# Performance work log

Measured on AMD Instinct MI355X. Metric: run time of the kernel, lower is better.

Reference implementation:

```python
import jax, jax.numpy as jnp
import numpy as np
import math

H = 1024
E = 16
ENT_STRENGTH = 0.5
COHERENCE_TIME = 10.0
TIME_STEP = 0.0
K = 2
# static list of rotation pairs (i<j), applied sequentially as in the torch double loop
PAIRS = np.array([(i, j) for i in range(E) for j in range(i + 1, E)], dtype=np.int32)


def _mlp(x, w1, b1, w2, b2):
    h = jax.nn.gelu(x @ w1 + b1, approximate=False)  # torch default GELU = exact erf
    return h @ w2 + b2


def _apply_entanglement(amps, ent):
    # sequential Givens rotations over expert pairs; carry shape [B,S,E]
    pairs = jnp.asarray(PAIRS)

    def step(carry, pair):
        i, j = pair[0], pair[1]
        angle = ent[i, j] * ENT_STRENGTH
        c, s = jnp.cos(angle), jnp.sin(angle)
        ai = jnp.take(carry, i, axis=-1)  # [B,S]
        aj = jnp.take(carry, j, axis=-1)
        oh_i = jax.nn.one_hot(i, E, dtype=carry.dtype)
        oh_j = jax.nn.one_hot(j, E, dtype=carry.dtype)
        new = (carry * (1.0 - oh_i - oh_j)
               + (c * ai - s * aj)[..., None] * oh_i
               + (s * ai + c * aj)[..., None] * oh_j)
        return new, None

    out, _ = jax.lax.scan(step, amps, pairs)
    return out


def setup_inputs() -> dict:
    key = jax.random.key(0)
    ks = jax.random.split(key, 10)
    sc1 = 1.0 / math.sqrt(H)
    sc2 = 1.0 / math.sqrt(H // 2)
    return {
        "hidden_states": jax.random.normal(ks[0], (4, 4096, H), dtype=jnp.float32),
        "w1a": jax.random.uniform(ks[1], (H, H // 2), jnp.float32, -sc1, sc1),
        "b1a": jnp.zeros((H // 2,), jnp.float32),
        "w2a": jax.random.uniform(ks[2], (H // 2, E), jnp.float32, -sc2, sc2),
        "b2a": jnp.zeros((E,), jnp.float32),
        "w1p": jax.random.uniform(ks[3], (H, H // 2), jnp.float32, -sc1, sc1),
        "b1p": jnp.zeros((H // 2,), jnp.float32),
        "w2p": jax.random.uniform(ks[4], (H // 2, E), jnp.float32, -sc2, sc2),
        "b2p": jnp.zeros((E,), jnp.float32),
        "ent": jax.random.normal(ks[5], (E, E), dtype=jnp.float32) * 0.1,
    }


def reference(hidden_states, w1a, b1a, w2a, b2a, w1p, b1p, w2p, b2p, ent):
    raw_amps = _mlp(hidden_states, w1a, b1a, w2a, b2a)                 # [B,S,E]
    raw_phases = jnp.tanh(_mlp(hidden_states, w1p, b1p, w2p, b2p)) * jnp.float32(math.pi)
    amplitudes = jnp.sqrt(jax.nn.softmax(jnp.abs(raw_amps), axis=-1))
    entangled = _apply_entanglement(amplitudes, ent)
    coherence = jnp.exp(jnp.float32(-TIME_STEP / COHERENCE_TIME))      # time_step buffer = 0 -> 1.0
    decoherent = entangled * coherence
    probs = decoherent ** 2
    probs = probs / jnp.maximum(jnp.sum(jnp.abs(probs), axis=-1, keepdims=True), 1e-12)
    top_p, top_i = jax.lax.top_k(probs, K)
    top_p = top_p / jnp.maximum(jnp.sum(jnp.abs(top_p), axis=-1, keepdims=True), 1e-12)
    return top_p, top_i, decoherent, raw_phases, probs
```

## Files before the change

kernel.cpp:

```cpp
#include <hip/hip_runtime.h>
#include <math.h>

#define NTOK   16384
#define HDIM   1024
#define HHALF  512
#define NE     16

#define OFF_TP  0
#define OFF_TI  (NTOK * 2)
#define OFF_DEC (NTOK * 4)
#define OFF_PH  (OFF_DEC + NTOK * NE)
#define OFF_PR  (OFF_PH + NTOK * NE)

typedef _Float16 half8 __attribute__((ext_vector_type(8)));
typedef _Float16 half4 __attribute__((ext_vector_type(4)));
typedef float f32x16 __attribute__((ext_vector_type(16)));
typedef float f32x4 __attribute__((ext_vector_type(4)));

#define LO_SCALE     2048.0f
#define LO_SCALE_INV (1.0f / 2048.0f)
#define MFMA32(a,b,c) __builtin_amdgcn_mfma_f32_32x32x16_f16(a,b,c,0,0,0)
#define MFMA16(a,b,c) __builtin_amdgcn_mfma_f32_16x16x32_f16(a,b,c,0,0,0)

#define BAR() asm volatile("s_waitcnt lgkmcnt(0)\n\ts_barrier" ::: "memory")

__device__ __forceinline__ float gelu_exact(float x) {
    return 0.5f * x * (1.0f + erff(x * 0.70710678118654752440f));
}

__device__ __forceinline__ void cvt_split(float4 v, half4& hi, half4& lo) {
    _Float16 h0 = (_Float16)v.x, h1 = (_Float16)v.y,
             h2 = (_Float16)v.z, h3 = (_Float16)v.w;
    hi = (half4){h0, h1, h2, h3};
    lo = (half4){(_Float16)((v.x - (float)h0) * LO_SCALE),
                 (_Float16)((v.y - (float)h1) * LO_SCALE),
                 (_Float16)((v.z - (float)h2) * LO_SCALE),
                 (_Float16)((v.w - (float)h3) * LO_SCALE)};
}

__global__ void __launch_bounds__(256)
qir_wtrans(const float* __restrict__ w1a, const float* __restrict__ w1p,
           _Float16* __restrict__ wt, float* __restrict__ out)
{
    int u = blockIdx.x * 256 + threadIdx.x;
    out[OFF_PH + u] = 0.0f;
    out[OFF_PH + 262144 + u] = 0.0f;

    int l  = u & 63;
    int f  = (u >> 6) & 7;
    int sl = (u >> 9) & 7;
    int kc = (u >> 12) & 31;
    int ph = u >> 17;
    int nf = f >> 2, kh = (f >> 1) & 1, pl = f & 1;
    int col = sl * 64 + nf * 32 + (l & 31);
    int k0  = kc * 32 + kh * 16 + (l >> 5) * 8;
    const float* __restrict__ W = ph ? w1p : w1a;
    half8 v;
    #pragma unroll
    for (int j = 0; j < 8; ++j) {
        float x = W[(size_t)(k0 + j) * HHALF + col];
        _Float16 h = (_Float16)x;
        v[j] = pl ? (_Float16)((x - (float)h) * LO_SCALE) : h;
    }
    *(half8*)&wt[(size_t)u * 8] = v;
}

__device__ __forceinline__ void kstep(
    int kc, const float* __restrict__ aptr, const _Float16* __restrict__ bptr,
    char* Acur, char* Anxt, int a_rd, int a_off0, int a_off1,
    half8 (&Bc)[4], half8 (&Bn)[4],
    float4 (&xw)[2], float4 (&xl)[2],
    f32x16 (&am)[4], f32x16 (&cm)[4])
{
    if (kc + 2 < 32) {
        xl[0] = *(const float4*)(aptr + (kc + 2) * 32);
        xl[1] = *(const float4*)(aptr + (kc + 2) * 32 + 16);
    }
    if (kc + 1 < 32) {
        #pragma unroll
        for (int j = 0; j < 4; ++j)
            Bn[j] = *(const half8*)(bptr + (size_t)(kc + 1) * 32768 + j * 512);
    }
    #pragma unroll
    for (int kh = 0; kh < 2; ++kh) {
        const char* Ah = Acur + kh * 4096 + a_rd;
        half8 ah[4], al[4];
        #pragma unroll
        for (int mf = 0; mf < 4; ++mf) {
            ah[mf] = *(const half8*)(Ah + mf * 512);
            al[mf] = *(const half8*)(Ah + 8192 + mf * 512);
        }
        half8 bh = Bc[kh * 2], bl = Bc[kh * 2 + 1];
        #pragma unroll
        for (int mf = 0; mf < 4; ++mf) {
            am[mf] = MFMA32(ah[mf], bh, am[mf]);
            cm[mf] = MFMA32(al[mf], bh, cm[mf]);
            cm[mf] = MFMA32(ah[mf], bl, cm[mf]);
        }
    }
    if (kc + 1 < 32) {
        half4 hv, lv;
        cvt_split(xw[0], hv, lv);
        *(half4*)(Anxt + a_off0) = hv; *(half4*)(Anxt + a_off0 + 8192) = lv;
        cvt_split(xw[1], hv, lv);
        *(half4*)(Anxt + a_off1) = hv; *(half4*)(Anxt + a_off1 + 8192) = lv;
    }
    BAR();
}

__global__ void __launch_bounds__(512, 2)
qir_gemm(const float* __restrict__ xg, const _Float16* __restrict__ wt,
         const float* __restrict__ b1a, const float* __restrict__ w2a, const float* __restrict__ b2a,
         const float* __restrict__ b1p, const float* __restrict__ w2p, const float* __restrict__ b2p,
         float* __restrict__ out)
{
    extern __shared__ char smem[];
    const int tid = threadIdx.x;
    const int l  = tid & 63;
    const int w  = tid >> 6;
    const int bid  = blockIdx.x;
    const int mblk = bid & 127;
    const int v    = bid >> 7;
    const int ph   = v & 1;
    const int nh   = v >> 1;
    const int tok0 = mblk * 128;

    const float* __restrict__ b1 = ph ? b1p : b1a;
    const float* __restrict__ w2 = ph ? w2p : w2a;
    const float* __restrict__ b2 = ph ? b2p : b2a;
    const _Float16* __restrict__ wtp = wt + ((size_t)ph << 20);

    char* const Ab0 = smem;
    char* const Ab1 = smem + 16384;

    const int r  = tid >> 2;
    const int kq = tid & 3;
    const float* __restrict__ aptr = xg + (size_t)(tok0 + r) * HDIM + kq * 4;
    const int a_off0 = (kq >> 1) * 2048 + r * 16 + (kq & 1) * 8;
    const int a_off1 = a_off0 + 4096;
    const int a_rd = (l >> 5) * 2048 + (l & 31) * 16;

    const int c32 = nh * 8 + w;
    const _Float16* __restrict__ bptr =
        wtp + (c32 >> 1) * 4096 + (c32 & 1) * 2048 + (size_t)l * 8;

    f32x16 am[4], cm[4];
    #pragma unroll
    for (int mf = 0; mf < 4; ++mf)
        #pragma unroll
        for (int rg = 0; rg < 16; ++rg) { am[mf][rg] = 0.f; cm[mf][rg] = 0.f; }

    half8 Bc[4], Bn[4];
    float4 xw[2], xl[2];

    {
        float4 v0 = *(const float4*)(aptr);
        float4 v1 = *(const float4*)(aptr + 16);
        half4 hv, lv;
        cvt_split(v0, hv, lv);
        *(half4*)(Ab0 + a_off0) = hv; *(half4*)(Ab0 + a_off0 + 8192) = lv;
        cvt_split(v1, hv, lv);
        *(half4*)(Ab0 + a_off1) = hv; *(half4*)(Ab0 + a_off1 + 8192) = lv;
    }
    #pragma unroll
    for (int j = 0; j < 4; ++j) Bc[j] = *(const half8*)(bptr + j * 512);
    xw[0] = *(const float4*)(aptr + 32);
    xw[1] = *(const float4*)(aptr + 48);
    BAR();

    for (int kk = 0; kk < 16; ++kk) {
        kstep(2 * kk,     aptr, bptr, Ab0, Ab1, a_rd, a_off0, a_off1,
              Bc, Bn, xw, xl, am, cm);
        kstep(2 * kk + 1, aptr, bptr, Ab1, Ab0, a_rd, a_off0, a_off1,
              Bn, Bc, xl, xw, am, cm);
    }

    const float bb = b1[nh * 256 + w * 32 + (l & 31)];
    #pragma unroll
    for (int mf = 0; mf < 4; ++mf)
        #pragma unroll
        for (int rg = 0; rg < 16; ++rg)
            am[mf][rg] = gelu_exact(am[mf][rg] + cm[mf][rg] * LO_SCALE_INV + bb);

    char* const Hw = smem + w * 5120;

    half8 w2h, w2l;
    #pragma unroll
    for (int j = 0; j < 8; ++j) {
        int kg = nh * 256 + w * 32 + (l >> 4) * 8 + j;
        float vv = w2[(size_t)kg * NE + (l & 15)];
        _Float16 hh = (_Float16)vv;
        w2h[j] = hh;
        w2l[j] = (_Float16)((vv - (float)hh) * LO_SCALE);
    }

    f32x4 acc2[2][4], acc2s[2][4];
    #pragma unroll
    for (int p2 = 0; p2 < 2; ++p2)
        #pragma unroll
        for (int m16 = 0; m16 < 4; ++m16)
            #pragma unroll
            for (int rg = 0; rg < 4; ++rg) { acc2[p2][m16][rg] = 0.f; acc2s[p2][m16][rg] = 0.f; }

    #pragma unroll
    for (int p2 = 0; p2 < 2; ++p2) {
        #pragma unroll
        for (int fr = 0; fr < 2; ++fr)
            #pragma unroll
            for (int rg = 0; rg < 16; ++rg) {
                int row = fr * 32 + (rg & 3) + 8 * (rg >> 2) + 4 * (l >> 5);
                float vv = am[p2 * 2 + fr][rg];
                *(_Float16*)(Hw + row * 80 + (l & 31) * 2) = (_Float16)vv;
            }
        #pragma unroll
        for (int m16 = 0; m16 < 4; ++m16) {
            half8 a2 = *(const half8*)(Hw + (m16 * 16 + (l & 15)) * 80 + (l >> 4) * 16);
            acc2[p2][m16]  = MFMA16(a2, w2h, acc2[p2][m16]);
            acc2s[p2][m16] = MFMA16(a2, w2l, acc2s[p2][m16]);
        }
        #pragma unroll
        for (int fr = 0; fr < 2; ++fr)
            #pragma unroll
            for (int rg = 0; rg < 16; ++rg) {
                int row = fr * 32 + (rg & 3) + 8 * (rg >> 2) + 4 * (l >> 5);
                float vv = am[p2 * 2 + fr][rg];
                _Float16 hh = (_Float16)vv;
                *(_Float16*)(Hw + row * 80 + (l & 31) * 2) = (_Float16)(vv - (float)hh);
            }
        #pragma unroll
        for (int m16 = 0; m16 < 4; ++m16) {
            half8 a2 = *(const half8*)(Hw + (m16 * 16 + (l & 15)) * 80 + (l >> 4) * 16);
            acc2[p2][m16] = MFMA16(a2, w2h, acc2[p2][m16]);
        }
    }

    __syncthreads();
    float* const P = (float*)smem;
    #pragma unroll
    for (int p2 = 0; p2 < 2; ++p2)
        #pragma unroll
        for (int m16 = 0; m16 < 4; ++m16)
            #pragma unroll
            for (int rg = 0; rg < 4; ++rg) {
                int t = p2 * 64 + m16 * 16 + ((l >> 4) << 2) + rg;
                P[w * 2048 + t * 16 + (l & 15)] =
                    acc2[p2][m16][rg] + acc2s[p2][m16][rg] * LO_SCALE_INV;
            }
    __syncthreads();

    #pragma unroll
    for (int rep = 0; rep < 4; ++rep) {
        int oi = tid + rep * 512;
        int t = oi >> 4, e = oi & 15;
        float sum = 0.5f * b2[e];
        #pragma unroll
        for (int w8 = 0; w8 < 8; ++w8) sum += P[w8 * 2048 + t * 16 + e];
        atomicAdd(out + (ph ? OFF_PH : OFF_PR) + (size_t)(tok0 + t) * NE + e, sum);
    }
}

__global__ void __launch_bounds__(512)
qir_mlp(const float* __restrict__ xg,
        const float* __restrict__ w1a, const float* __restrict__ b1a,
        const float* __restrict__ w2a, const float* __restrict__ b2a,
        const float* __restrict__ w1p, const float* __restrict__ b1p,
        const float* __restrict__ w2p, const float* __restrict__ b2p,
        float* __restrict__ out)
{
    __shared__ float sh_w[16][HHALF];
    __shared__ float sh_x[16][68];

    const int tid  = threadIdx.x;
    const int cg   = tid & 63;
    const int tg   = tid >> 6;
    const int tok0 = blockIdx.x * 64;
    const int cA   = cg * 4;
    const int cB   = 256 + cg * 4;

    for (int phase = 0; phase < 2; ++phase) {
        const float* __restrict__ w1 = phase ? w1p : w1a;
        const float* __restrict__ b1 = phase ? b1p : b1a;
        const float* __restrict__ w2 = phase ? w2p : w2a;
        const float* __restrict__ b2 = phase ? b2p : b2a;

        float acc[8][8];
        #pragma unroll
        for (int t = 0; t < 8; ++t)
            #pragma unroll
            for (int c = 0; c < 8; ++c) acc[t][c] = 0.0f;

        float4 wreg[4];
        float4 xreg = make_float4(0.f, 0.f, 0.f, 0.f);

        auto load_chunk = [&](int kc) {
            #pragma unroll
            for (int p = 0; p < 4; ++p) {
                int f  = tid + p * 512;
                int k  = f >> 7;
                int c4 = (f & 127) << 2;
                wreg[p] = *(const float4*)&w1[(kc * 16 + k) * HHALF + c4];
            }
            if (tid < 256) {
                int t  = tid >> 2;
                int k4 = (tid & 3) << 2;
                xreg = *(const float4*)&xg[(size_t)(tok0 + t) * HDIM + kc * 16 + k4];
            }
        };

        load_chunk(0);
        for (int kc = 0; kc < HDIM / 16; ++kc) {
            __syncthreads();
            #pragma unroll
            for (int p = 0; p < 4; ++p) {
                int f  = tid + p * 512;
                int k  = f >> 7;
                int c4 = (f & 127) << 2;
                *(float4*)&sh_w[k][c4] = wreg[p];
            }
            if (tid < 256) {
                int t  = tid >> 2;
                int k4 = (tid & 3) << 2;
                sh_x[k4 + 0][t] = xreg.x;
                sh_x[k4 + 1][t] = xreg.y;
                sh_x[k4 + 2][t] = xreg.z;
                sh_x[k4 + 3][t] = xreg.w;
            }
            __syncthreads();
            if (kc + 1 < HDIM / 16) load_chunk(kc + 1);

            #pragma unroll 4
            for (int k = 0; k < 16; ++k) {
                float4 xa = *(const float4*)&sh_x[k][tg * 8];
                float4 xb = *(const float4*)&sh_x[k][tg * 8 + 4];
                float4 wa = *(const float4*)&sh_w[k][cA];
                float4 wb = *(const float4*)&sh_w[k][cB];
                float xs[8] = {xa.x, xa.y, xa.z, xa.w, xb.x, xb.y, xb.z, xb.w};
                float ws[8] = {wa.x, wa.y, wa.z, wa.w, wb.x, wb.y, wb.z, wb.w};
                #pragma unroll
                for (int t = 0; t < 8; ++t)
                    #pragma unroll
                    for (int c = 0; c < 8; ++c)
                        acc[t][c] = fmaf(xs[t], ws[c], acc[t][c]);
            }
        }

        {
            float4 bA4 = *(const float4*)&b1[cA];
            float4 bB4 = *(const float4*)&b1[cB];
            float bs[8] = {bA4.x, bA4.y, bA4.z, bA4.w, bB4.x, bB4.y, bB4.z, bB4.w};
            #pragma unroll
            for (int t = 0; t < 8; ++t)
                #pragma unroll
                for (int c = 0; c < 8; ++c)
                    acc[t][c] = gelu_exact(acc[t][c] + bs[c]);
        }

        for (int e = 0; e < NE; ++e) {
            float w2v[8];
            #pragma unroll
            for (int j = 0; j < 4; ++j) {
                w2v[j]     = w2[(cA + j) * NE + e];
                w2v[4 + j] = w2[(cB + j) * NE + e];
            }
            float bias2 = b2[e];
            #pragma unroll
            for (int t = 0; t < 8; ++t) {
                float s = 0.0f;
                #pragma unroll
                for (int j = 0; j < 8; ++j) s = fmaf(acc[t][j], w2v[j], s);
                #pragma unroll
                for (int off = 1; off < 64; off <<= 1)
                    s += __shfl_xor(s, off, 64);
                if (cg == 0) {
                    float raw   = s + bias2;
                    int   token = tok0 + tg * 8 + t;
                    out[(phase ? OFF_PH : OFF_PR) + (size_t)token * NE + e] = raw;
                }
            }
        }
    }
}

__global__ void __launch_bounds__(256)
qir_epilogue(const float* __restrict__ ent, float* __restrict__ out)
{
    __shared__ float sh_c[120], sh_s[120];
    const int tid = threadIdx.x;
    if (tid < 120) {
        int rem = tid, i = 0;
        while (rem >= 15 - i) { rem -= 15 - i; ++i; }
        int j = i + 1 + rem;
        float ang = ent[i * NE + j] * 0.5f;
        sh_c[tid] = cosf(ang);
        sh_s[tid] = sinf(ang);
    }
    __syncthreads();

    const int token = blockIdx.x * 256 + tid;

    #pragma unroll
    for (int q = 0; q < 4; ++q) {
        float4 v = *(const float4*)&out[OFF_PH + (size_t)token * NE + q * 4];
        v.x = tanhf(v.x) * 3.14159265358979323846f;
        v.y = tanhf(v.y) * 3.14159265358979323846f;
        v.z = tanhf(v.z) * 3.14159265358979323846f;
        v.w = tanhf(v.w) * 3.14159265358979323846f;
        *(float4*)&out[OFF_PH + (size_t)token * NE + q * 4] = v;
    }

    float a[16];
    #pragma unroll
    for (int q = 0; q < 4; ++q) {
        float4 v = *(const float4*)&out[OFF_PR + (size_t)token * NE + q * 4];
        a[q*4+0] = v.x; a[q*4+1] = v.y; a[q*4+2] = v.z; a[q*4+3] = v.w;
    }

    float m = fabsf(a[0]);
    #pragma unroll
    for (int e = 1; e < 16; ++e) m = fmaxf(m, fabsf(a[e]));
    float ssum = 0.0f;
    #pragma unroll
    for (int e = 0; e < 16; ++e) { a[e] = expf(fabsf(a[e]) - m); ssum += a[e]; }
    float inv = 1.0f / ssum;
    #pragma unroll
    for (int e = 0; e < 16; ++e) a[e] = sqrtf(a[e] * inv);

    {
        int p = 0;
        #pragma unroll
        for (int i = 0; i < 16; ++i) {
            #pragma unroll
            for (int j = i + 1; j < 16; ++j) {
                float c = sh_c[p], s = sh_s[p]; ++p;
                float ai = a[i], aj = a[j];
                a[i] = c * ai - s * aj;
                a[j] = s * ai + c * aj;
            }
        }
    }

    #pragma unroll
    for (int q = 0; q < 4; ++q)
        *(float4*)&out[OFF_DEC + (size_t)token * NE + q * 4] =
            make_float4(a[q*4], a[q*4+1], a[q*4+2], a[q*4+3]);

    float pr[16];
    float s2 = 0.0f;
    #pragma unroll
    for (int e = 0; e < 16; ++e) { pr[e] = a[e] * a[e]; s2 += pr[e]; }
    float inv2 = 1.0f / fmaxf(s2, 1e-12f);
    #pragma unroll
    for (int e = 0; e < 16; ++e) pr[e] *= inv2;
    #pragma unroll
    for (int q = 0; q < 4; ++q)
        *(float4*)&out[OFF_PR + (size_t)token * NE + q * 4] =
            make_float4(pr[q*4], pr[q*4+1], pr[q*4+2], pr[q*4+3]);

    float bv = pr[0]; int bi = 0;
    #pragma unroll
    for (int e = 1; e < 16; ++e) if (pr[e] > bv) { bv = pr[e]; bi = e; }
    float sv = -1.0f; int si = 0;
    #pragma unroll
    for (int e = 0; e < 16; ++e) if (e != bi && pr[e] > sv) { sv = pr[e]; si = e; }
    float ts = fmaxf(fabsf(bv) + fabsf(sv), 1e-12f);
    out[OFF_TP + (size_t)token * 2 + 0] = bv / ts;
    out[OFF_TP + (size_t)token * 2 + 1] = sv / ts;
    out[OFF_TI + (size_t)token * 2 + 0] = (float)bi;
    out[OFF_TI + (size_t)token * 2 + 1] = (float)si;
}

extern "C" void kernel_launch(void* const* d_in, const int* in_sizes, int n_in,
                              void* d_out, int out_size, void* d_ws, size_t ws_size,
                              hipStream_t stream) {
    const float* xg  = (const float*)d_in[0];
    const float* w1a = (const float*)d_in[1];
    const float* b1a = (const float*)d_in[2];
    const float* w2a = (const float*)d_in[3];
    const float* b2a = (const float*)d_in[4];
    const float* w1p = (const float*)d_in[5];
    const float* b1p = (const float*)d_in[6];
    const float* w2p = (const float*)d_in[7];
    const float* b2p = (const float*)d_in[8];
    const float* ent = (const float*)d_in[9];
    float* out = (float*)d_out;

    if (ws_size >= (size_t)4 * 1024 * 1024) {
        _Float16* wt = (_Float16*)d_ws;
        qir_wtrans<<<1024, 256, 0, stream>>>(w1a, w1p, wt, out);
        qir_gemm<<<512, 512, 65536, stream>>>(xg, wt, b1a, w2a, b2a,
                                              b1p, w2p, b2p, out);
    } else {
        qir_mlp<<<NTOK / 64, 512, 0, stream>>>(xg, w1a, b1a, w2a, b2a,
                                               w1p, b1p, w2p, b2p, out);
    }
    qir_epilogue<<<NTOK / 256, 256, 0, stream>>>(ent, out);
}
```

Baseline: 120.8 us.

## Fuse epilogue into GEMM with full-N tiles and bf16 low-part split

The GEMM is reorganised so each block covers 32 tokens and the full 512-wide hidden dimension of one MLP branch. This removes the N-split, the atomicAdd reduction, the zero-init pass and the separate epilogue kernel; softmax, the Givens rotations, normalisation and top-2 now run inside the GEMM block. The fp32 emulation also changes: the weight low part is stored as bf16 and accumulated into a single scaled accumulator, rather than kept in a separate correction accumulator. In exchange, only 32 threads per block do the serial epilogue, and the new mixed f16/bf16 split may change accuracy.

After: 137.0 us. 1.13x slower.

```diff
diff --git a/kernel.cpp b/kernel.cpp
--- a/kernel.cpp
+++ b/kernel.cpp
@@ -5,6 +5,7 @@
 #define HDIM   1024
 #define HHALF  512
 #define NE     16
+#define PI_F   3.14159265358979323846f
 
 #define OFF_TP  0
 #define OFF_TI  (NTOK * 2)
@@ -14,38 +15,33 @@
 
 typedef _Float16 half8 __attribute__((ext_vector_type(8)));
 typedef _Float16 half4 __attribute__((ext_vector_type(4)));
+typedef short    bf8   __attribute__((ext_vector_type(8)));
+typedef short    bf4   __attribute__((ext_vector_type(4)));
 typedef float f32x16 __attribute__((ext_vector_type(16)));
 typedef float f32x4 __attribute__((ext_vector_type(4)));
 
-#define LO_SCALE     2048.0f
-#define LO_SCALE_INV (1.0f / 2048.0f)
-#define MFMA32(a,b,c) __builtin_amdgcn_mfma_f32_32x32x16_f16(a,b,c,0,0,0)
-#define MFMA16(a,b,c) __builtin_amdgcn_mfma_f32_16x16x32_f16(a,b,c,0,0,0)
+#define SCALE      2048.0f
+#define SCALE_INV  (1.0f / 2048.0f)
+#define MFMA_F16(a,b,c)  __builtin_amdgcn_mfma_f32_32x32x16_f16(a,b,c,0,0,0)
+#define MFMA_BF16(a,b,c) __builtin_amdgcn_mfma_f32_32x32x16_bf16(a,b,c,0,0,0)
+#define MFMA16(a,b,c)    __builtin_amdgcn_mfma_f32_16x16x32_f16(a,b,c,0,0,0)
 
 #define BAR() asm volatile("s_waitcnt lgkmcnt(0)\n\ts_barrier" ::: "memory")
 
 __device__ __forceinline__ float gelu_exact(float x) {
     return 0.5f * x * (1.0f + erff(x * 0.70710678118654752440f));
 }
-
-__device__ __forceinline__ void cvt_split(float4 v, half4& hi, half4& lo) {
-    _Float16 h0 = (_Float16)v.x, h1 = (_Float16)v.y,
-             h2 = (_Float16)v.z, h3 = (_Float16)v.w;
-    hi = (half4){h0, h1, h2, h3};
-    lo = (half4){(_Float16)((v.x - (float)h0) * LO_SCALE),
-                 (_Float16)((v.y - (float)h1) * LO_SCALE),
-                 (_Float16)((v.z - (float)h2) * LO_SCALE),
-                 (_Float16)((v.w - (float)h3) * LO_SCALE)};
+__device__ __forceinline__ short f32_to_bf16_bits(float f) {
+    unsigned u = __builtin_bit_cast(unsigned, f);
+    u += 0x7FFFu + ((u >> 16) & 1u);
+    return (short)(u >> 16);
 }
 
 __global__ void __launch_bounds__(256)
 qir_wtrans(const float* __restrict__ w1a, const float* __restrict__ w1p,
-           _Float16* __restrict__ wt, float* __restrict__ out)
+           short* __restrict__ wt)
 {
     int u = blockIdx.x * 256 + threadIdx.x;
-    out[OFF_PH + u] = 0.0f;
-    out[OFF_PH + 262144 + u] = 0.0f;
-
     int l  = u & 63;
     int f  = (u >> 6) & 7;
     int sl = (u >> 9) & 7;
@@ -55,207 +51,284 @@
     int col = sl * 64 + nf * 32 + (l & 31);
     int k0  = kc * 32 + kh * 16 + (l >> 5) * 8;
     const float* __restrict__ W = ph ? w1p : w1a;
-    half8 v;
+    bf8 v;
     #pragma unroll
     for (int j = 0; j < 8; ++j) {
         float x = W[(size_t)(k0 + j) * HHALF + col];
         _Float16 h = (_Float16)x;
-        v[j] = pl ? (_Float16)((x - (float)h) * LO_SCALE) : h;
-    }
-    *(half8*)&wt[(size_t)u * 8] = v;
-}
-
-__device__ __forceinline__ void kstep(
-    int kc, const float* __restrict__ aptr, const _Float16* __restrict__ bptr,
-    char* Acur, char* Anxt, int a_rd, int a_off0, int a_off1,
-    half8 (&Bc)[4], half8 (&Bn)[4],
-    float4 (&xw)[2], float4 (&xl)[2],
-    f32x16 (&am)[4], f32x16 (&cm)[4])
-{
-    if (kc + 2 < 32) {
-        xl[0] = *(const float4*)(aptr + (kc + 2) * 32);
-        xl[1] = *(const float4*)(aptr + (kc + 2) * 32 + 16);
-    }
-    if (kc + 1 < 32) {
-        #pragma unroll
-        for (int j = 0; j < 4; ++j)
-            Bn[j] = *(const half8*)(bptr + (size_t)(kc + 1) * 32768 + j * 512);
-    }
-    #pragma unroll
-    for (int kh = 0; kh < 2; ++kh) {
-        const char* Ah = Acur + kh * 4096 + a_rd;
-        half8 ah[4], al[4];
-        #pragma unroll
-        for (int mf = 0; mf < 4; ++mf) {
-            ah[mf] = *(const half8*)(Ah + mf * 512);
-            al[mf] = *(const half8*)(Ah + 8192 + mf * 512);
-        }
-        half8 bh = Bc[kh * 2], bl = Bc[kh * 2 + 1];
-        #pragma unroll
-        for (int mf = 0; mf < 4; ++mf) {
-            am[mf] = MFMA32(ah[mf], bh, am[mf]);
-            cm[mf] = MFMA32(al[mf], bh, cm[mf]);
-            cm[mf] = MFMA32(ah[mf], bl, cm[mf]);
-        }
-    }
-    if (kc + 1 < 32) {
-        half4 hv, lv;
-        cvt_split(xw[0], hv, lv);
-        *(half4*)(Anxt + a_off0) = hv; *(half4*)(Anxt + a_off0 + 8192) = lv;
-        cvt_split(xw[1], hv, lv);
-        *(half4*)(Anxt + a_off1) = hv; *(half4*)(Anxt + a_off1 + 8192) = lv;
-    }
-    BAR();
-}
-
-__global__ void __launch_bounds__(512, 2)
-qir_gemm(const float* __restrict__ xg, const _Float16* __restrict__ wt,
+        v[j] = pl ? f32_to_bf16_bits(x - (float)h)
+                  : __builtin_bit_cast(short, h);
+    }
+    *(bf8*)&wt[(size_t)u * 8] = v;
+}
+
+__global__ void __launch_bounds__(256, 2)
+qir_gemm(const float* __restrict__ xg, const short* __restrict__ wt,
          const float* __restrict__ b1a, const float* __restrict__ w2a, const float* __restrict__ b2a,
          const float* __restrict__ b1p, const float* __restrict__ w2p, const float* __restrict__ b2p,
-         float* __restrict__ out)
+         const float* __restrict__ ent, float* __restrict__ out)
 {
     extern __shared__ char smem[];
     const int tid = threadIdx.x;
     const int l  = tid & 63;
     const int w  = tid >> 6;
     const int bid  = blockIdx.x;
-    const int mblk = bid & 127;
-    const int v    = bid >> 7;
-    const int ph   = v & 1;
-    const int nh   = v >> 1;
-    const int tok0 = mblk * 128;
+    const int mblk = bid & 511;
+    const int ph   = bid >> 9;
+    const int tok0 = mblk * 32;
 
     const float* __restrict__ b1 = ph ? b1p : b1a;
     const float* __restrict__ w2 = ph ? w2p : w2a;
     const float* __restrict__ b2 = ph ? b2p : b2a;
-    const _Float16* __restrict__ wtp = wt + ((size_t)ph << 20);
+    const short* __restrict__ wtp = wt + ((size_t)ph << 20);
+
+    float* const cs = (float*)(smem + 16384);
+    float* const sn = cs + 120;
+    if (tid < 120) {
+        int rem = tid, i = 0;
+        while (rem >= 15 - i) { rem -= 15 - i; ++i; }
+        int j = i + 1 + rem;
+        float ang = ent[i * NE + j] * 0.5f;
+        cs[tid] = cosf(ang);
+        sn[tid] = sinf(ang);
+    }
+
+    const int r  = tid >> 3;
+    const int kq = tid & 7;
+    const float* __restrict__ aptr = xg + (size_t)(tok0 + r) * HDIM + kq * 4;
+    const int a_w  = ((kq >> 2) * 2 + ((kq >> 1) & 1)) * 3 * 512 + r * 16 + (kq & 1) * 8;
+    const int a_rd = (l >> 5) * 3 * 512 + (l & 31) * 16;
+
+    f32x16 acc[4];
+    #pragma unroll
+    for (int g = 0; g < 4; ++g)
+        #pragma unroll
+        for (int rg = 0; rg < 16; ++rg) acc[g][rg] = 0.0f;
+
+    half8 Bch[4], Bdh[4];
+    bf8   Bcl[4], Bdl[4];
+    float4 xw, xl4;
+
+#define BOFF(KC, KH, G, PL) \
+    ((((size_t)((KC) * 8 + (2 * w + ((G) >> 1))) * 8) + ((G) & 1) * 4 + (KH) * 2 + (PL)) * 512 + (size_t)l * 8)
+
+    auto stageA = [&](char* buf, float4 v) {
+        _Float16 h0 = (_Float16)v.x, h1 = (_Float16)v.y,
+                 h2 = (_Float16)v.z, h3 = (_Float16)v.w;
+        const _Float16 S = (_Float16)SCALE;
+        half4 hi = {(_Float16)(h0 * S), (_Float16)(h1 * S),
+                    (_Float16)(h2 * S), (_Float16)(h3 * S)};
+        half4 lo = {(_Float16)((v.x - (float)h0) * SCALE),
+                    (_Float16)((v.y - (float)h1) * SCALE),
+                    (_Float16)((v.z - (float)h2) * SCALE),
+                    (_Float16)((v.w - (float)h3) * SCALE)};
+        bf4 hb = {f32_to_bf16_bits((float)h0 * SCALE),
+                  f32_to_bf16_bits((float)h1 * SCALE),
+                  f32_to_bf16_bits((float)h2 * SCALE),
+                  f32_to_bf16_bits((float)h3 * SCALE)};
+        *(half4*)(buf + a_w)        = hi;
+        *(half4*)(buf + a_w + 512)  = lo;
+        *(bf4*)  (buf + a_w + 1024) = hb;
+    };
 
     char* const Ab0 = smem;
-    char* const Ab1 = smem + 16384;
-
-    const int r  = tid >> 2;
-    const int kq = tid & 3;
-    const float* __restrict__ aptr = xg + (size_t)(tok0 + r) * HDIM + kq * 4;
-    const int a_off0 = (kq >> 1) * 2048 + r * 16 + (kq & 1) * 8;
-    const int a_off1 = a_off0 + 4096;
-    const int a_rd = (l >> 5) * 2048 + (l & 31) * 16;
-
-    const int c32 = nh * 8 + w;
-    const _Float16* __restrict__ bptr =
-        wtp + (c32 >> 1) * 4096 + (c32 & 1) * 2048 + (size_t)l * 8;
-
-    f32x16 am[4], cm[4];
-    #pragma unroll
-    for (int mf = 0; mf < 4; ++mf)
-        #pragma unroll
-        for (int rg = 0; rg < 16; ++rg) { am[mf][rg] = 0.f; cm[mf][rg] = 0.f; }
-
-    half8 Bc[4], Bn[4];
-    float4 xw[2], xl[2];
-
-    {
-        float4 v0 = *(const float4*)(aptr);
-        float4 v1 = *(const float4*)(aptr + 16);
-        half4 hv, lv;
-        cvt_split(v0, hv, lv);
-        *(half4*)(Ab0 + a_off0) = hv; *(half4*)(Ab0 + a_off0 + 8192) = lv;
-        cvt_split(v1, hv, lv);
-        *(half4*)(Ab0 + a_off1) = hv; *(half4*)(Ab0 + a_off1 + 8192) = lv;
-    }
-    #pragma unroll
-    for (int j = 0; j < 4; ++j) Bc[j] = *(const half8*)(bptr + j * 512);
-    xw[0] = *(const float4*)(aptr + 32);
-    xw[1] = *(const float4*)(aptr + 48);
+    char* const Ab1 = smem + 6144;
+
+    stageA(Ab0, *(const float4*)aptr);
+    #pragma unroll
+    for (int g = 0; g < 4; ++g) {
+        Bch[g] = *(const half8*)&wtp[BOFF(0, 0, g, 0)];
+        Bcl[g] = *(const bf8*)  &wtp[BOFF(0, 0, g, 1)];
+    }
+    xw = *(const float4*)(aptr + 32);
     BAR();
 
+    auto kstep = [&](int kc, char* Acur, char* Anxt, float4& xcur, float4& xnxt) {
+        #pragma unroll
+        for (int g = 0; g < 4; ++g) {
+            Bdh[g] = *(const half8*)&wtp[BOFF(kc, 1, g, 0)];
+            Bdl[g] = *(const bf8*)  &wtp[BOFF(kc, 1, g, 1)];
+        }
+        if (kc + 2 < 32) xnxt = *(const float4*)(aptr + (kc + 2) * 32);
+
+        {
+            const char* A0 = Acur + a_rd;
+            half8 xh = *(const half8*)(A0);
+            half8 xl = *(const half8*)(A0 + 512);
+            bf8   xb = *(const bf8*)  (A0 + 1024);
+            #pragma unroll
+            for (int g = 0; g < 4; ++g) {
+                acc[g] = MFMA_F16(xh, Bch[g], acc[g]);
+                acc[g] = MFMA_F16(xl, Bch[g], acc[g]);
+                acc[g] = MFMA_BF16(xb, Bcl[g], acc[g]);
+            }
+        }
+        if (kc + 1 < 32) {
+            #pragma unroll
+            for (int g = 0; g < 4; ++g) {
+                Bch[g] = *(const half8*)&wtp[BOFF(kc + 1, 0, g, 0)];
+                Bcl[g] = *(const bf8*)  &wtp[BOFF(kc + 1, 0, g, 1)];
+            }
+        }
+        {
+            const char* A1 = Acur + 3072 + a_rd;
+            half8 xh = *(const half8*)(A1);
+            half8 xl = *(const half8*)(A1 + 512);
+            bf8   xb = *(const bf8*)  (A1 + 1024);
+            #pragma unroll
+            for (int g = 0; g < 4; ++g) {
+                acc[g] = MFMA_F16(xh, Bdh[g], acc[g]);
+                acc[g] = MFMA_F16(xl, Bdh[g], acc[g]);
+                acc[g] = MFMA_BF16(xb, Bdl[g], acc[g]);
+            }
+        }
+        if (kc + 1 < 32) stageA(Anxt, xcur);
+        BAR();
+    };
+
     for (int kk = 0; kk < 16; ++kk) {
-        kstep(2 * kk,     aptr, bptr, Ab0, Ab1, a_rd, a_off0, a_off1,
-              Bc, Bn, xw, xl, am, cm);
-        kstep(2 * kk + 1, aptr, bptr, Ab1, Ab0, a_rd, a_off0, a_off1,
-              Bn, Bc, xl, xw, am, cm);
-    }
-
-    const float bb = b1[nh * 256 + w * 32 + (l & 31)];
-    #pragma unroll
-    for (int mf = 0; mf < 4; ++mf)
+        kstep(2 * kk,     Ab0, Ab1, xw, xl4);
+        kstep(2 * kk + 1, Ab1, Ab0, xl4, xw);
+    }
+#undef BOFF
+
+    #pragma unroll
+    for (int g = 0; g < 4; ++g) {
+        const float bb = b1[w * 128 + g * 32 + (l & 31)];
         #pragma unroll
         for (int rg = 0; rg < 16; ++rg)
-            am[mf][rg] = gelu_exact(am[mf][rg] + cm[mf][rg] * LO_SCALE_INV + bb);
-
-    char* const Hw = smem + w * 5120;
-
-    half8 w2h, w2l;
-    #pragma unroll
-    for (int j = 0; j < 8; ++j) {
-        int kg = nh * 256 + w * 32 + (l >> 4) * 8 + j;
-        float vv = w2[(size_t)kg * NE + (l & 15)];
-        _Float16 hh = (_Float16)vv;
-        w2h[j] = hh;
-        w2l[j] = (_Float16)((vv - (float)hh) * LO_SCALE);
-    }
-
-    f32x4 acc2[2][4], acc2s[2][4];
-    #pragma unroll
-    for (int p2 = 0; p2 < 2; ++p2)
-        #pragma unroll
-        for (int m16 = 0; m16 < 4; ++m16)
-            #pragma unroll
-            for (int rg = 0; rg < 4; ++rg) { acc2[p2][m16][rg] = 0.f; acc2s[p2][m16][rg] = 0.f; }
-
-    #pragma unroll
-    for (int p2 = 0; p2 < 2; ++p2) {
-        #pragma unroll
-        for (int fr = 0; fr < 2; ++fr)
-            #pragma unroll
-            for (int rg = 0; rg < 16; ++rg) {
-                int row = fr * 32 + (rg & 3) + 8 * (rg >> 2) + 4 * (l >> 5);
-                float vv = am[p2 * 2 + fr][rg];
-                *(_Float16*)(Hw + row * 80 + (l & 31) * 2) = (_Float16)vv;
-            }
-        #pragma unroll
-        for (int m16 = 0; m16 < 4; ++m16) {
-            half8 a2 = *(const half8*)(Hw + (m16 * 16 + (l & 15)) * 80 + (l >> 4) * 16);
-            acc2[p2][m16]  = MFMA16(a2, w2h, acc2[p2][m16]);
-            acc2s[p2][m16] = MFMA16(a2, w2l, acc2s[p2][m16]);
-        }
-        #pragma unroll
-        for (int fr = 0; fr < 2; ++fr)
-            #pragma unroll
-            for (int rg = 0; rg < 16; ++rg) {
-                int row = fr * 32 + (rg & 3) + 8 * (rg >> 2) + 4 * (l >> 5);
-                float vv = am[p2 * 2 + fr][rg];
-                _Float16 hh = (_Float16)vv;
-                *(_Float16*)(Hw + row * 80 + (l & 31) * 2) = (_Float16)(vv - (float)hh);
-            }
-        #pragma unroll
-        for (int m16 = 0; m16 < 4; ++m16) {
-            half8 a2 = *(const half8*)(Hw + (m16 * 16 + (l & 15)) * 80 + (l >> 4) * 16);
-            acc2[p2][m16] = MFMA16(a2, w2h, acc2[p2][m16]);
-        }
-    }
-
+            acc[g][rg] = gelu_exact(acc[g][rg] * SCALE_INV + bb);
+    }
+
+    char* const Hw = smem + w * 2048;
+    char* const hb = Hw + ((l >> 3) & 3) * 512 + (l & 7) * 2;
+    float* const P = (float*)(smem + 8192);
+
+    f32x4 acc2[2], acc2s[2];
+    #pragma unroll
+    for (int m16 = 0; m16 < 2; ++m16)
+        #pragma unroll
+        for (int rg = 0; rg < 4; ++rg) { acc2[m16][rg] = 0.f; acc2s[m16][rg] = 0.f; }
+
+    #pragma unroll
+    for (int g = 0; g < 4; ++g) {
+        half8 w2h, w2l;
+        #pragma unroll
+        for (int j = 0; j < 8; ++j) {
+            int kg = w * 128 + g * 32 + (l >> 4) * 8 + j;
+            float vv = w2[(size_t)kg * NE + (l & 15)];
+            _Float16 hh = (_Float16)vv;
+            w2h[j] = hh;
+            w2l[j] = (_Float16)((vv - (float)hh) * SCALE);
+        }
+        #pragma unroll
+        for (int rg = 0; rg < 16; ++rg) {
+            int row0 = (rg & 3) + 8 * (rg >> 2) + 4 * (l >> 5);
+            *(_Float16*)(hb + row0 * 16) = (_Float16)acc[g][rg];
+        }
+        #pragma unroll
+        for (int m16 = 0; m16 < 2; ++m16) {
+            half8 a2 = *(const half8*)(Hw + (l >> 4) * 512 +
+                                       (m16 * 16 + (l & 15)) * 16);
+            acc2[m16]  = MFMA16(a2, w2h, acc2[m16]);
+            acc2s[m16] = MFMA16(a2, w2l, acc2s[m16]);
+        }
+        #pragma unroll
+        for (int rg = 0; rg < 16; ++rg) {
+            int row0 = (rg & 3) + 8 * (rg >> 2) + 4 * (l >> 5);
+            float vv = acc[g][rg];
+            _Float16 hh = (_Float16)vv;
+            *(_Float16*)(hb + row0 * 16) = (_Float16)(vv - (float)hh);
+        }
+        #pragma unroll
+        for (int m16 = 0; m16 < 2; ++m16) {
+            half8 a2 = *(const half8*)(Hw + (l >> 4) * 512 +
+                                       (m16 * 16 + (l & 15)) * 16);
+            acc2[m16] = MFMA16(a2, w2h, acc2[m16]);
+        }
+    }
+
+    #pragma unroll
+    for (int m16 = 0; m16 < 2; ++m16)
+        #pragma unroll
+        for (int rg = 0; rg < 4; ++rg) {
+            int row = m16 * 16 + ((l >> 4) << 2) + rg;
+            P[w * 512 + row * 16 + (l & 15)] =
+                acc2[m16][rg] + acc2s[m16][rg] * SCALE_INV;
+        }
     __syncthreads();
-    float* const P = (float*)smem;
-    #pragma unroll
-    for (int p2 = 0; p2 < 2; ++p2)
-        #pragma unroll
-        for (int m16 = 0; m16 < 4; ++m16)
-            #pragma unroll
-            for (int rg = 0; rg < 4; ++rg) {
-                int t = p2 * 64 + m16 * 16 + ((l >> 4) << 2) + rg;
-                P[w * 2048 + t * 16 + (l & 15)] =
-                    acc2[p2][m16][rg] + acc2s[p2][m16][rg] * LO_SCALE_INV;
-            }
-    __syncthreads();
-
-    #pragma unroll
-    for (int rep = 0; rep < 4; ++rep) {
-        int oi = tid + rep * 512;
+
+    #pragma unroll
+    for (int rep = 0; rep < 2; ++rep) {
+        int oi = tid + rep * 256;
         int t = oi >> 4, e = oi & 15;
-        float sum = 0.5f * b2[e];
-        #pragma unroll
-        for (int w8 = 0; w8 < 8; ++w8) sum += P[w8 * 2048 + t * 16 + e];
-        atomicAdd(out + (ph ? OFF_PH : OFF_PR) + (size_t)(tok0 + t) * NE + e, sum);
+        float sum = b2[e]
+                  + P[t * 16 + e] + P[512 + t * 16 + e]
+                  + P[1024 + t * 16 + e] + P[1536 + t * 16 + e];
+        if (ph) out[OFF_PH + (size_t)(tok0 + t) * NE + e] = tanhf(sum) * PI_F;
+        else    P[t * 16 + e] = sum;
+    }
+
+    if (!ph) {
+        __syncthreads();
+        if (tid < 32) {
+            const int token = tok0 + tid;
+            float a[16];
+            #pragma unroll
+            for (int e = 0; e < 16; ++e) a[e] = P[tid * 16 + e];
+
+            float m = fabsf(a[0]);
+            #pragma unroll
+            for (int e = 1; e < 16; ++e) m = fmaxf(m, fabsf(a[e]));
+            float ssum = 0.0f;
+            #pragma unroll
+            for (int e = 0; e < 16; ++e) { a[e] = expf(fabsf(a[e]) - m); ssum += a[e]; }
+            float inv = 1.0f / ssum;
+            #pragma unroll
+            for (int e = 0; e < 16; ++e) a[e] = sqrtf(a[e] * inv);
+
+            {
+                int p = 0;
+                #pragma unroll
+                for (int i = 0; i < 16; ++i)
+                    #pragma unroll
+                    for (int j = i + 1; j < 16; ++j) {
+                        float c = cs[p], s = sn[p]; ++p;
+                        float ai = a[i], aj = a[j];
+                        a[i] = c * ai - s * aj;
+                        a[j] = s * ai + c * aj;
+                    }
+            }
+
+            #pragma unroll
+            for (int q = 0; q < 4; ++q)
+                *(float4*)&out[OFF_DEC + (size_t)token * NE + q * 4] =
+                    make_float4(a[q*4], a[q*4+1], a[q*4+2], a[q*4+3]);
+
+            float pr[16];
+            float s2 = 0.0f;
+            #pragma unroll
+            for (int e = 0; e < 16; ++e) { pr[e] = a[e] * a[e]; s2 += pr[e]; }
+            float inv2 = 1.0f / fmaxf(s2, 1e-12f);
+            #pragma unroll
+            for (int e = 0; e < 16; ++e) pr[e] *= inv2;
+            #pragma unroll
+            for (int q = 0; q < 4; ++q)
+                *(float4*)&out[OFF_PR + (size_t)token * NE + q * 4] =
+                    make_float4(pr[q*4], pr[q*4+1], pr[q*4+2], pr[q*4+3]);
+
+            float bv = pr[0]; int bi = 0;
+            #pragma unroll
+            for (int e = 1; e < 16; ++e) if (pr[e] > bv) { bv = pr[e]; bi = e; }
+            float sv = -1.0f; int si = 0;
+            #pragma unroll
+            for (int e = 0; e < 16; ++e) if (e != bi && pr[e] > sv) { sv = pr[e]; si = e; }
+            float ts = fmaxf(fabsf(bv) + fabsf(sv), 1e-12f);
+            out[OFF_TP + (size_t)token * 2 + 0] = bv / ts;
+            out[OFF_TP + (size_t)token * 2 + 1] = sv / ts;
+            out[OFF_TI + (size_t)token * 2 + 0] = (float)bi;
+            out[OFF_TI + (size_t)token * 2 + 1] = (float)si;
+        }
     }
 }
 
@@ -401,10 +474,10 @@
     #pragma unroll
     for (int q = 0; q < 4; ++q) {
         float4 v = *(const float4*)&out[OFF_PH + (size_t)token * NE + q * 4];
-        v.x = tanhf(v.x) * 3.14159265358979323846f;
-        v.y = tanhf(v.y) * 3.14159265358979323846f;
-        v.z = tanhf(v.z) * 3.14159265358979323846f;
-        v.w = tanhf(v.w) * 3.14159265358979323846f;
+        v.x = tanhf(v.x) * PI_F;
+        v.y = tanhf(v.y) * PI_F;
+        v.z = tanhf(v.z) * PI_F;
+        v.w = tanhf(v.w) * PI_F;
         *(float4*)&out[OFF_PH + (size_t)token * NE + q * 4] = v;
     }
 
@@ -485,13 +558,13 @@
     float* out = (float*)d_out;
 
     if (ws_size >= (size_t)4 * 1024 * 1024) {
-        _Float16* wt = (_Float16*)d_ws;
-        qir_wtrans<<<1024, 256, 0, stream>>>(w1a, w1p, wt, out);
-        qir_gemm<<<512, 512, 65536, stream>>>(xg, wt, b1a, w2a, b2a,
-                                              b1p, w2p, b2p, out);
+        short* wt = (short*)d_ws;
+        qir_wtrans<<<1024, 256, 0, stream>>>(w1a, w1p, wt);
+        qir_gemm<<<1024, 256, 17408, stream>>>(xg, wt, b1a, w2a, b2a,
+                                               b1p, w2p, b2p, ent, out);
     } else {
         qir_mlp<<<NTOK / 64, 512, 0, stream>>>(xg, w1a, b1a, w2a, b2a,
                                                w1p, b1p, w2p, b2p, out);
-    }
-    qir_epilogue<<<NTOK / 256, 256, 0, stream>>>(ent, out);
-}
+        qir_epilogue<<<NTOK / 256, 256, 0, stream>>>(ent, out);
+    }
+}
```
